# Kernel tuning notes

Measured on AMD Instinct MI355X. Metric: run time of the kernel, lower is better.

## Reference

```python
import jax, jax.numpy as jnp
import numpy as np

RADIUS = 2
TEMP = 1.0
B, CIN, D, H, W = 1, 32, 64, 64, 64
PROJ, OUT = 64, 64
K = (2 * RADIUS + 1) ** 3  # 125 local offsets

_OFFSETS = np.array([(dz, dy, dx)
                     for dz in range(-RADIUS, RADIUS + 1)
                     for dy in range(-RADIUS, RADIUS + 1)
                     for dx in range(-RADIUS, RADIUS + 1)], dtype=np.int32)


def _conv3d(x, w, b, pad):
    y = jax.lax.conv_general_dilated(
        x, w, window_strides=(1, 1, 1), padding=[(pad, pad)] * 3,
        dimension_numbers=('NCDHW', 'OIDHW', 'NCDHW'))
    if b is not None:
        y = y + b[None, :, None, None, None]
    return y


def _l2norm(x):
    # torch F.normalize(dim=1): x / max(||x||_2, 1e-12)
    n = jnp.sqrt(jnp.sum(x * x, axis=1, keepdims=True))
    return x / jnp.maximum(n, 1e-12)


def _inorm(x, eps=1e-5):
    # InstanceNorm3d (affine=False): normalize over spatial dims per (B,C)
    mu = jnp.mean(x, axis=(2, 3, 4), keepdims=True)
    var = jnp.mean((x - mu) ** 2, axis=(2, 3, 4), keepdims=True)
    return (x - mu) * jax.lax.rsqrt(var + eps)


def _ntn(x):
    return jnp.nan_to_num(x, nan=0.0, posinf=0.0, neginf=0.0)


def setup_inputs() -> dict:
    key = jax.random.key(0)
    ks = jax.random.split(key, 8)
    s = 0.05
    return {
        'source_features': jax.random.normal(ks[0], (B, CIN, D, H, W), jnp.float32),
        'warped_target_features': jax.random.normal(ks[1], (B, CIN, D, H, W), jnp.float32),
        'w_src': jax.random.normal(ks[2], (PROJ, CIN, 1, 1, 1), jnp.float32) * s,
        'b_src': jnp.zeros((PROJ,), jnp.float32),
        'w_tgt': jax.random.normal(ks[3], (PROJ, CIN, 1, 1, 1), jnp.float32) * s,
        'b_tgt': jnp.zeros((PROJ,), jnp.float32),
        'w_enc1': jax.random.normal(ks[4], (OUT, K + 5, 3, 3, 3), jnp.float32) * s,
        'b_enc1': jnp.zeros((OUT,), jnp.float32),
        'w_enc2': jax.random.normal(ks[5], (OUT, OUT, 3, 3, 3), jnp.float32) * s,
        'b_enc2': jnp.zeros((OUT,), jnp.float32),
    }


def reference(source_features, warped_target_features, w_src, b_src, w_tgt, b_tgt,
              w_enc1, b_enc1, w_enc2, b_enc2):
    sp = _l2norm(_conv3d(source_features, w_src, b_src, 0))      # [B,P,D,H,W]
    tp = _l2norm(_conv3d(warped_target_features, w_tgt, b_tgt, 0))
    pt = jnp.pad(tp, ((0, 0), (0, 0), (RADIUS, RADIUS), (RADIUS, RADIUS), (RADIUS, RADIUS)),
                 mode='edge')  # replicate pad

    starts = jnp.asarray(_OFFSETS + RADIUS, jnp.int32)  # [K,3] slice starts

    def corr_one(st):
        sh = jax.lax.dynamic_slice(pt, (0, 0, st[0], st[1], st[2]), (B, PROJ, D, H, W))
        return jnp.sum(sp * sh, axis=1)  # [B,D,H,W]

    corr = jnp.transpose(jax.vmap(corr_one)(starts), (1, 0, 2, 3, 4))  # [B,K,D,H,W]
    scaled = corr / max(TEMP, 1e-6)

    top2 = jax.lax.top_k(jnp.moveaxis(scaled, 1, -1), 2)[0]  # [B,D,H,W,2]
    m = jnp.moveaxis(top2[..., 0:1], -1, 1)   # running max   [B,1,D,H,W]
    s2 = jnp.moveaxis(top2[..., 1:2], -1, 1)  # second max

    p = jnp.exp(scaled - m)                    # [B,K,D,H,W]
    Z = jnp.sum(p, axis=1, keepdims=True)
    inv = 1.0 / jnp.maximum(Z, 1e-8)

    offv = jnp.asarray(_OFFSETS, jnp.float32)  # [K,3]
    expected_offset = _ntn(jnp.einsum('bkdhw,kc->bcdhw', p, offv) * inv)
    confidence = _ntn(jnp.minimum(inv, 1.0))   # max-prob = exp(m-m)/Z
    second_prob = jnp.exp(s2 - m) * inv
    margin = _ntn(jnp.maximum(confidence - second_prob, 0.0))
    entropy = _ntn(m + jnp.log(jnp.maximum(Z, 1e-8))
                   - jnp.sum(p * scaled, axis=1, keepdims=True) * inv)

    enc_in = jnp.concatenate([corr, expected_offset, confidence, entropy], axis=1)  # [B,K+5,D,H,W]
    h = _conv3d(enc_in, w_enc1, b_enc1, 1)
    h = jax.nn.gelu(_inorm(h), approximate=False)
    h = _conv3d(h, w_enc2, b_enc2, 1)
    h = jax.nn.gelu(_inorm(h), approximate=False)
    encoded_features = _ntn(h)

    return expected_offset, confidence, margin, entropy, encoded_features
```

## Files before the change

### kernel.cpp

```cpp
#include <hip/hip_runtime.h>

#define DEV __device__ __forceinline__

typedef short bf16x8 __attribute__((ext_vector_type(8)));
typedef float f32x4 __attribute__((ext_vector_type(4)));

static const int NVOX = 262144;

DEV float bflo(unsigned int u) { return __uint_as_float(u << 16); }
DEV float bfhi(unsigned int u) { return __uint_as_float(u & 0xffff0000u); }
DEV float bf2f(unsigned short s) { return __uint_as_float(((unsigned int)s) << 16); }
DEV unsigned short f2bf(float f) {
    unsigned int x = __float_as_uint(f);
    x += 0x7fffu + ((x >> 16) & 1u);
    return (unsigned short)(x >> 16);
}
DEV float ldin(const void* p, int i, int f) {
    return f ? ((const float*)p)[i] : bf2f(((const unsigned short*)p)[i]);
}

DEV void gld16(const unsigned short* g, unsigned short* l) {
    __builtin_amdgcn_global_load_lds(
        (const __attribute__((address_space(1))) unsigned int*)g,
        (__attribute__((address_space(3))) unsigned int*)l, 16, 0, 0);
}

__global__ void sniff_kernel(const unsigned short* __restrict__ src, int* __restrict__ flag) {
    __shared__ int cnt[256];
    int t = threadIdx.x;
    int c = 0;
    for (int i = t; i < 4096; i += 256) {
        unsigned int u = (unsigned int)src[i] & 0x7fffu;
        c += (u >= 0x4900u) ? 1 : 0;
    }
    cnt[t] = c;
    __syncthreads();
    for (int s = 128; s > 0; s >>= 1) {
        if (t < s) cnt[t] += cnt[t + s];
        __syncthreads();
    }
    if (t == 0) *flag = (cnt[0] > 8) ? 1 : 0;
}

__global__ void prep_kernel(const void* __restrict__ w1, const void* __restrict__ w2,
                            const void* __restrict__ bsv, const void* __restrict__ btv,
                            const void* __restrict__ b1v, const void* __restrict__ b2v,
                            const int* __restrict__ flag,
                            unsigned short* __restrict__ Wf1,
                            unsigned short* __restrict__ Wf2,
                            float* __restrict__ fbias) {
    const int f = *flag;
    int idx = blockIdx.x * 256 + threadIdx.x;
    const int N1  = 27 * 4 * 4 * 512;
    const int N1E = 2 * 4 * 512;
    const int N2  = 27 * 2 * 4 * 512;
    if (idx < N1) {
        int frag = idx >> 9;
        int r    = idx & 511;
        int lane = r >> 3, j = r & 7;
        int nt = frag & 3;
        int tk = frag >> 2;
        int tap = tk >> 2, kc = tk & 3;
        int o  = nt * 16 + (lane & 15);
        int cp = kc * 32 + (lane >> 4) * 8 + j;
        Wf1[idx] = f2bf(ldin(w1, (o * 130 + cp) * 27 + tap, f));
    } else if (idx < N1 + N1E) {
        int i2 = idx - N1;
        int frag = i2 >> 9;
        int r    = i2 & 511;
        int lane = r >> 3, j = r & 7;
        int nt = frag & 3, kc = frag >> 2;
        int o   = nt * 16 + (lane & 15);
        int kap = kc * 32 + (lane >> 4) * 8 + j;
        unsigned short val = 0;
        if (kap < 54) {
            int tap = kap >> 1, ch = 128 + (kap & 1);
            val = f2bf(ldin(w1, (o * 130 + ch) * 27 + tap, f));
        }
        Wf1[idx] = val;
    } else if (idx < N1 + N1E + N2) {
        int i2 = idx - N1 - N1E;
        int frag = i2 >> 9;
        int r    = i2 & 511;
        int lane = r >> 3, j = r & 7;
        int nt = frag & 3;
        int tk = frag >> 2;
        int tap = tk >> 1, kc = tk & 1;
        int o = nt * 16 + (lane & 15);
        int c = kc * 32 + (lane >> 4) * 8 + j;
        Wf2[i2] = f2bf(ldin(w2, (o * 64 + c) * 27 + tap, f));
    } else if (idx < N1 + N1E + N2 + 256) {
        int j = idx - N1 - N1E - N2;
        const void* bp = (j < 64) ? bsv : (j < 128) ? btv : (j < 192) ? b1v : b2v;
        fbias[j] = ldin(bp, j & 63, f);
    }
}

__global__ __launch_bounds__(256) void proj_kernel(
        const void* __restrict__ Xsrc, const void* __restrict__ Xtgt,
        const void* __restrict__ Wsrc, const void* __restrict__ Wtgt,
        const float* __restrict__ fbias, const int* __restrict__ flag,
        unsigned short* __restrict__ SP, unsigned short* __restrict__ TP) {
    const int f = *flag;
    const void* Xin = blockIdx.y ? Xtgt : Xsrc;
    const void* W   = blockIdx.y ? Wtgt : Wsrc;
    const float* Bb = fbias + (blockIdx.y ? 64 : 0);
    unsigned short* Outp = blockIdx.y ? TP : SP;

    __shared__ float ws[2048];
    const int t = threadIdx.x;
    for (int i = t; i < 2048; i += 256) {
        int ci = i >> 6, o = i & 63;
        ws[i] = ldin(W, o * 32 + ci, f);
    }
    __syncthreads();

    const size_t v = (size_t)blockIdx.x * 256 + t;
    float acc[64];
#pragma unroll
    for (int o = 0; o < 64; ++o) acc[o] = Bb[o];
    if (f) {
        const float* Xf = (const float*)Xin;
        for (int ci = 0; ci < 32; ++ci) {
            float x = Xf[(size_t)ci * NVOX + v];
            const float4* wr = (const float4*)(ws + ci * 64);
#pragma unroll
            for (int o4 = 0; o4 < 16; ++o4) {
                float4 w4 = wr[o4];
                acc[o4 * 4 + 0] = fmaf(w4.x, x, acc[o4 * 4 + 0]);
                acc[o4 * 4 + 1] = fmaf(w4.y, x, acc[o4 * 4 + 1]);
                acc[o4 * 4 + 2] = fmaf(w4.z, x, acc[o4 * 4 + 2]);
                acc[o4 * 4 + 3] = fmaf(w4.w, x, acc[o4 * 4 + 3]);
            }
        }
    } else {
        const unsigned short* Xb = (const unsigned short*)Xin;
        for (int ci = 0; ci < 32; ++ci) {
            float x = bf2f(Xb[(size_t)ci * NVOX + v]);
            const float4* wr = (const float4*)(ws + ci * 64);
#pragma unroll
            for (int o4 = 0; o4 < 16; ++o4) {
                float4 w4 = wr[o4];
                acc[o4 * 4 + 0] = fmaf(w4.x, x, acc[o4 * 4 + 0]);
                acc[o4 * 4 + 1] = fmaf(w4.y, x, acc[o4 * 4 + 1]);
                acc[o4 * 4 + 2] = fmaf(w4.z, x, acc[o4 * 4 + 2]);
                acc[o4 * 4 + 3] = fmaf(w4.w, x, acc[o4 * 4 + 3]);
            }
        }
    }
    float s = 0.f;
#pragma unroll
    for (int o = 0; o < 64; ++o) s = fmaf(acc[o], acc[o], s);
    float scale = 1.f / fmaxf(sqrtf(s), 1e-12f);

    unsigned int pk[32];
#pragma unroll
    for (int o = 0; o < 32; ++o)
        pk[o] = (unsigned int)f2bf(acc[2 * o] * scale) |
                ((unsigned int)f2bf(acc[2 * o + 1] * scale) << 16);
    uint4* outp = (uint4*)(Outp + v * 64);
#pragma unroll
    for (int j = 0; j < 8; ++j)
        outp[j] = make_uint4(pk[4 * j], pk[4 * j + 1], pk[4 * j + 2], pk[4 * j + 3]);
}

__global__ __launch_bounds__(256) void corr_kernel(
        const unsigned short* __restrict__ SP, const unsigned short* __restrict__ TP,
        unsigned short* __restrict__ X1, float* __restrict__ Out) {
    __shared__ __align__(16) unsigned short tpb[2][80 * 64];
    __shared__ __align__(16) unsigned short stage[64 * 128];

    const int t = threadIdx.x;
    const int wv = t >> 6, lane = t & 63;
    const int q = lane >> 4, l16 = lane & 15;
    const int x0 = wv * 16;

    const int bid = blockIdx.x;
    const int wg = (bid & 7) * 512 + (bid >> 3);
    const int z = wg >> 6, y = wg & 63;
    const size_t vbase = ((size_t)z * 64 + y) * 64;

    const unsigned short* arow = SP + (vbase + x0 + l16) * 64 + q * 8;
    const bf16x8 a0 = *(const bf16x8*)(arow);
    const bf16x8 a1 = *(const bf16x8*)(arow + 32);

    auto stage_tp = [&](int it, int b) {
        const int zc = min(max(z + it / 5 - 2, 0), 63);
        const int yc = min(max(y + it % 5 - 2, 0), 63);
        const unsigned short* tb = TP + ((size_t)zc * 64 + yc) * 4096;
#pragma unroll
        for (int j = 0; j < 2; ++j) {
            int c = t + j * 256;
            int pp = c >> 3, cc = c & 7;
            int xc = min(max(pp - 2, 0), 63);
            gld16(tb + xc * 64 + ((cc ^ (pp & 7)) * 8),
                  &tpb[b][(wv * 64 + j * 256) * 8]);
        }
        if (wv < 2) {
            int c = 512 + wv * 64 + lane;
            int pp = c >> 3, cc = c & 7;
            int xc = min(max(pp - 2, 0), 63);
            gld16(tb + xc * 64 + ((cc ^ (pp & 7)) * 8),
                  &tpb[b][(512 + wv * 64) * 8]);
        }
    };

    stage_tp(0, 0);
    __syncthreads();

    int p = 0;
    for (int it = 0; it < 25; ++it) {
        if (it < 24) stage_tp(it + 1, p ^ 1);

        f32x4 acc[2] = {{0.f, 0.f, 0.f, 0.f}, {0.f, 0.f, 0.f, 0.f}};
        {
            const char* tb = (const char*)tpb[p];
#pragma unroll
            for (int nt = 0; nt < 2; ++nt) {
                const int pr = x0 + nt * 16 + l16;
                bf16x8 b0 = *(const bf16x8*)(tb + pr * 128 + ((q ^ (pr & 7)) * 16));
                bf16x8 b1 = *(const bf16x8*)(tb + pr * 128 + (((4 + q) ^ (pr & 7)) * 16));
                acc[nt] = __builtin_amdgcn_mfma_f32_16x16x32_bf16(a0, b0, acc[nt], 0, 0, 0);
                acc[nt] = __builtin_amdgcn_mfma_f32_16x16x32_bf16(a1, b1, acc[nt], 0, 0, 0);
            }
        }
        const int kb = it * 5;
        char* sg = (char*)stage;
#pragma unroll
        for (int nt = 0; nt < 2; ++nt) {
#pragma unroll
            for (int r = 0; r < 4; ++r) {
                int ml = q * 4 + r;
                int dxp = nt * 16 + l16 - ml;
                if ((unsigned)dxp < 5u) {
                    int xl = x0 + ml;
                    *(unsigned short*)(sg + xl * 256 + (((kb + dxp) * 2) ^ ((xl & 7) << 4))) =
                        f2bf(acc[nt][r]);
                }
            }
        }
        __syncthreads();
        p ^= 1;
    }

    {
        const int vox = t >> 2, part = t & 3;
        const int sx = (vox & 7) << 4;
        const char* sg = (const char*)stage;
        uint4 u[4];
#pragma unroll
        for (int j = 0; j < 4; ++j)
            u[j] = *(const uint4*)(sg + vox * 256 + ((part * 64 + j * 16) ^ sx));

        float m = -1e30f, s2 = -1e30f;
#pragma unroll
        for (int j = 0; j < 4; ++j) {
            const unsigned int uu[4] = {u[j].x, u[j].y, u[j].z, u[j].w};
#pragma unroll
            for (int w = 0; w < 4; ++w) {
                int k = part * 32 + j * 8 + w * 2;
                float d0 = (k < 125) ? bflo(uu[w]) : -1e30f;
                float d1 = (k + 1 < 125) ? bfhi(uu[w]) : -1e30f;
                float lo0 = fminf(d0, m); m = fmaxf(d0, m); s2 = fmaxf(s2, lo0);
                float lo1 = fminf(d1, m); m = fmaxf(d1, m); s2 = fmaxf(s2, lo1);
            }
        }
#pragma unroll
        for (int off = 1; off <= 2; off <<= 1) {
            float om = __shfl_xor(m, off, 64);
            float os = __shfl_xor(s2, off, 64);
            float lo = fminf(m, om);
            m = fmaxf(m, om);
            s2 = fmaxf(fmaxf(s2, os), lo);
        }
        int kk = part * 32;
        int dz0 = kk / 25, rem = kk - dz0 * 25, dy0 = rem / 5, dx0 = rem - dy0 * 5;
        float fx = (float)(dx0 - 2), fy = (float)(dy0 - 2), fz = (float)(dz0 - 2);
        float Zs = 0.f, S1 = 0.f, Ox = 0.f, Oy = 0.f, Oz = 0.f;
#pragma unroll
        for (int j = 0; j < 4; ++j) {
            const unsigned int uu[4] = {u[j].x, u[j].y, u[j].z, u[j].w};
#pragma unroll
            for (int w = 0; w < 8; ++w) {
                int k = part * 32 + j * 8 + w;
                bool ok = (k < 125);
                float d = (w & 1) ? bfhi(uu[w >> 1]) : bflo(uu[w >> 1]);
                d = ok ? d : 0.f;
                float e = ok ? __expf(d - m) : 0.f;
                Zs += e; S1 = fmaf(e, d, S1);
                Ox = fmaf(e, fx, Ox); Oy = fmaf(e, fy, Oy); Oz = fmaf(e, fz, Oz);
                fx += 1.f;
                if (fx > 2.5f) { fx = -2.f; fy += 1.f; if (fy > 2.5f) { fy = -2.f; fz += 1.f; } }
            }
        }
#pragma unroll
        for (int off = 1; off <= 2; off <<= 1) {
            Zs += __shfl_xor(Zs, off, 64);
            S1 += __shfl_xor(S1, off, 64);
            Ox += __shfl_xor(Ox, off, 64);
            Oy += __shfl_xor(Oy, off, 64);
            Oz += __shfl_xor(Oz, off, 64);
        }
        if (part == 0) {
            float inv  = 1.f / fmaxf(Zs, 1e-8f);
            float eoz = Oz * inv, eoy = Oy * inv, eox = Ox * inv;
            float conf = fminf(inv, 1.f);
            float marg = fmaxf(conf - __expf(s2 - m) * inv, 0.f);
            float ent  = m + __logf(fmaxf(Zs, 1e-8f)) - S1 * inv;
            char* sgw = (char*)stage;
            *(unsigned short*)(sgw + vox * 256 + (250 ^ sx)) = f2bf(eoz);
            *(unsigned short*)(sgw + vox * 256 + (252 ^ sx)) = f2bf(eoy);
            *(unsigned short*)(sgw + vox * 256 + (254 ^ sx)) = f2bf(eox);
            const size_t v = vbase + vox;
            *(unsigned int*)(X1 + v * 160 + 128) =
                (unsigned int)f2bf(conf) | ((unsigned int)f2bf(ent) << 16);
            Out[v]                    = eoz;
            Out[(size_t)NVOX + v]     = eoy;
            Out[(size_t)2 * NVOX + v] = eox;
            Out[(size_t)3 * NVOX + v] = conf;
            Out[(size_t)4 * NVOX + v] = marg;
            Out[(size_t)5 * NVOX + v] = ent;
        }
    }
    __syncthreads();

#pragma unroll
    for (int j = 0; j < 4; ++j) {
        int i = t + j * 256;
        int vox = i >> 4, cc = i & 15;
        *(uint4*)(X1 + (vbase + vox) * 160 + (size_t)cc * 8) =
            *(const uint4*)((const char*)stage + vox * 256 + ((cc * 16) ^ ((vox & 7) << 4)));
    }
}

template <int XSTRIDE, int CPAD, int KC, int NLD, int MINW, bool TAIL>
__global__ __launch_bounds__(256, MINW) void conv3_kernel(
        const unsigned short* __restrict__ Xin, const unsigned short* __restrict__ Wf,
        const unsigned short* __restrict__ Wfe,
        const float* __restrict__ Bias, unsigned short* __restrict__ Out) {
    constexpr int SLOT = 66 * CPAD;
    constexpr int CH16 = CPAD / 8;
    __shared__ __align__(16) unsigned short lds[3 * SLOT];
    const int lin = blockIdx.x;
    const int wg = (lin & 7) * 256 + (lin >> 3);
    const int z = wg >> 5;
    const int y = (wg & 31) * 2;
    const int t = threadIdx.x;
    const int wv = t >> 6, lane = t & 63;
    const int quad = lane >> 4, l16 = lane & 15;
    const int ml2 = (wv & 1) * 2;
    const int nt2 = (wv >> 1) * 2;

    f32x4 acc[2][2][2] = {};

    auto stage_plane = [&](int pidx) {
        const int zz = z + (pidx >> 2) - 1;
        const int py = y + (pidx & 3) - 1;
        if ((unsigned)zz >= 64u || (unsigned)py >= 64u) return;
        const unsigned short* base = Xin + (((size_t)zz * 64 + py) * 64) * XSTRIDE;
        unsigned short* dst = lds + (pidx % 3) * SLOT + CPAD;
#pragma unroll
        for (int i = 0; i < NLD; ++i) {
            int chunk = wv * 64 + lane + i * 256;
            int xi = chunk / CH16;
            int cc = chunk % CH16;
            gld16(base + xi * XSTRIDE + ((cc ^ ((xi + 1) & 7)) * 8),
                  dst + (size_t)(wv * 64 + i * 256) * 8);
        }
    };

    if (TAIL) {
        unsigned short* ebuf = lds;
#pragma unroll
        for (int i2 = 0; i2 < 16; ++i2) {
            int i = t + i2 * 256;
            int vox = i >> 5, slot = i & 31;
            unsigned int val = 0u;
            int kap;
            if (slot < 27) {
                int ddz = slot / 9 - 1, ddy = (slot / 3) % 3 - 1, dxx = slot % 3 - 1;
                int zz = z + ddz, yy = y + (vox >> 6) + ddy, xx = (vox & 63) + dxx;
                kap = slot * 2;
                if ((unsigned)zz < 64u && (unsigned)yy < 64u && (unsigned)xx < 64u)
                    val = *(const unsigned int*)(Xin + (((size_t)zz * 64 + yy) * 64 + xx) * XSTRIDE + 128);
            } else {
                kap = 54 + (slot - 27) * 2;
            }
            *(unsigned int*)(ebuf + (size_t)vox * 72 + kap) = val;
        }
        __syncthreads();
#pragma unroll
        for (int kc = 0; kc < 2; ++kc) {
            bf16x8 bte[2];
#pragma unroll
            for (int nl = 0; nl < 2; ++nl)
                bte[nl] = *(const bf16x8*)(Wfe + (size_t)(kc * 4 + nt2 + nl) * 512 + lane * 8);
#pragma unroll
            for (int r = 0; r < 2; ++r)
#pragma unroll
            for (int ml = 0; ml < 2; ++ml) {
                bf16x8 a = *(const bf16x8*)(ebuf + (size_t)(r * 64 + (ml2 + ml) * 16 + l16) * 72 + (kc * 4 + quad) * 8);
#pragma unroll
                for (int nl = 0; nl < 2; ++nl)
                    acc[r][ml][nl] = __builtin_amdgcn_mfma_f32_16x16x32_bf16(a, bte[nl], acc[r][ml][nl], 0, 0, 0);
            }
        }
        __syncthreads();
    }

    if (t < 6 * CH16) {
        int sl = t / (2 * CH16), r2 = (t / CH16) & 1, c = t % CH16;
        *(uint4*)(&lds[(size_t)sl * SLOT + (size_t)(r2 * 65) * CPAD + c * 8]) =
            make_uint4(0u, 0u, 0u, 0u);
    }
    stage_plane(0);
    stage_plane(1);
    __syncthreads();

    for (int i = 0; i < 9; ++i) {
        const int s0 = (i / 3) * 4 + i % 3;
        if (i == 3 || i == 6) {
            stage_plane(s0 + 1);
            stage_plane(s0 + 2);
            __syncthreads();
        } else if (s0 + 2 < 12) {
            stage_plane(s0 + 2);
        }

        const int zz = z + i / 3 - 1;
        const int dy = i % 3 - 1;
        const bool zok = (unsigned)zz < 64u;
        const bool rok0 = zok && (unsigned)(y + dy) < 64u;
        const bool rok1 = zok && (unsigned)(y + 1 + dy) < 64u;
        const unsigned short* sb0 = lds + (size_t)(s0 % 3) * SLOT;
        const unsigned short* sb1 = lds + (size_t)((s0 + 1) % 3) * SLOT;
        if (rok0 || rok1) {
#pragma unroll
            for (int dx = 0; dx < 3; ++dx) {
                const int tap = (i / 3) * 9 + (i % 3) * 3 + dx;
                const unsigned short* wt = Wf + ((size_t)tap * KC * 4) * 512 + lane * 8;
                bf16x8 bf[KC][2];
#pragma unroll
                for (int kc = 0; kc < KC; ++kc)
#pragma unroll
                    for (int nl = 0; nl < 2; ++nl)
                        bf[kc][nl] = *(const bf16x8*)(wt + (size_t)(kc * 4 + nt2 + nl) * 512);
#pragma unroll
                for (int kc = 0; kc < KC; ++kc) {
#pragma unroll
                    for (int ml = 0; ml < 2; ++ml) {
                        const int row = (ml2 + ml) * 16 + l16 + dx;
                        const int co = ((kc * 4 + quad) ^ (row & 7)) * 8;
                        if (rok0) {
                            bf16x8 a = *(const bf16x8*)(&sb0[(size_t)row * CPAD + co]);
#pragma unroll
                            for (int nl = 0; nl < 2; ++nl)
                                acc[0][ml][nl] = __builtin_amdgcn_mfma_f32_16x16x32_bf16(a, bf[kc][nl], acc[0][ml][nl], 0, 0, 0);
                        }
                        if (rok1) {
                            bf16x8 a = *(const bf16x8*)(&sb1[(size_t)row * CPAD + co]);
#pragma unroll
                            for (int nl = 0; nl < 2; ++nl)
                                acc[1][ml][nl] = __builtin_amdgcn_mfma_f32_16x16x32_bf16(a, bf[kc][nl], acc[1][ml][nl], 0, 0, 0);
                        }
                    }
                }
            }
        }
        __syncthreads();
    }

#pragma unroll
    for (int r = 0; r < 2; ++r) {
        const size_t vb = ((size_t)z * 64 + (y + r)) * 64;
#pragma unroll
        for (int ml = 0; ml < 2; ++ml) {
#pragma unroll
            for (int nl = 0; nl < 2; ++nl) {
                const int oc = (nt2 + nl) * 16 + l16;
                const float bv = Bias[oc];
#pragma unroll
                for (int rr = 0; rr < 4; ++rr)
                    Out[(vb + (ml2 + ml) * 16 + quad * 4 + rr) * 64 + oc] =
                        f2bf(acc[r][ml][nl][rr] + bv);
            }
        }
    }
}

__global__ __launch_bounds__(256) void stats_kernel(
        const unsigned short* __restrict__ H, float* __restrict__ stats) {
    const int t = threadIdx.x;
    const int c = t & 63, g = t >> 6;
    float s = 0.f, q = 0.f;
    for (int v = blockIdx.x * 4 + g; v < NVOX; v += gridDim.x * 4) {
        float x = bf2f(H[(size_t)v * 64 + c]);
        s += x; q = fmaf(x, x, q);
    }
    __shared__ float ls[256], lq[256];
    ls[t] = s; lq[t] = q;
    __syncthreads();
    if (t < 64) {
        s = ls[t] + ls[t + 64] + ls[t + 128] + ls[t + 192];
        q = lq[t] + lq[t + 64] + lq[t + 128] + lq[t + 192];
        atomicAdd(&stats[c], s);
        atomicAdd(&stats[64 + c], q);
    }
}

__global__ void finalize_kernel(const float* __restrict__ stats, float* __restrict__ musr) {
    int c = threadIdx.x;
    if (c < 64) {
        float mu  = stats[c] * (1.0f / 262144.0f);
        float var = stats[64 + c] * (1.0f / 262144.0f) - mu * mu;
        musr[c] = mu;
        musr[64 + c] = rsqrtf(var + 1e-5f);
    }
}

__global__ __launch_bounds__(256) void norm_gelu_kernel(
        const unsigned short* __restrict__ H, const float* __restrict__ musr,
        unsigned short* __restrict__ G) {
    const size_t base = ((size_t)blockIdx.x * 256 + threadIdx.x) * 8;
    uint4 u = *(const uint4*)(H + base);
    const int c0 = (int)(base & 63);
    const unsigned int uu[4] = {u.x, u.y, u.z, u.w};
    unsigned int w[4];
#pragma unroll
    for (int p = 0; p < 4; ++p) {
        int c = c0 + p * 2;
        float x0 = (bflo(uu[p]) - musr[c]) * musr[64 + c];
        float x1 = (bfhi(uu[p]) - musr[c + 1]) * musr[64 + c + 1];
        float g0 = 0.5f * x0 * (1.f + erff(x0 * 0.70710678118f));
        float g1 = 0.5f * x1 * (1.f + erff(x1 * 0.70710678118f));
        w[p] = (unsigned int)f2bf(g0) | ((unsigned int)f2bf(g1) << 16);
    }
    *(uint4*)(G + base) = make_uint4(w[0], w[1], w[2], w[3]);
}

__global__ __launch_bounds__(256) void out_final_kernel(
        const unsigned short* __restrict__ H2, const float* __restrict__ musr,
        float* __restrict__ OutEnc) {
    __shared__ float tile[64 * 260];
    const int t = threadIdx.x;
    const size_t v0 = (size_t)blockIdx.x * 256;
#pragma unroll
    for (int i = 0; i < 8; ++i) {
        int chunk = t + i * 256;
        uint4 u = *(const uint4*)(H2 + v0 * 64 + (size_t)chunk * 8);
        int vox = chunk >> 3;
        int c0 = (chunk & 7) * 8;
        const unsigned int uu[4] = {u.x, u.y, u.z, u.w};
#pragma unroll
        for (int p = 0; p < 4; ++p) {
            int c = c0 + p * 2;
            float x0 = (bflo(uu[p]) - musr[c]) * musr[64 + c];
            float x1 = (bfhi(uu[p]) - musr[c + 1]) * musr[64 + c + 1];
            tile[c * 260 + vox]       = 0.5f * x0 * (1.f + erff(x0 * 0.70710678118f));
            tile[(c + 1) * 260 + vox] = 0.5f * x1 * (1.f + erff(x1 * 0.70710678118f));
        }
    }
    __syncthreads();
    const int c = t >> 2, sub = t & 3;
#pragma unroll
    for (int iter = 0; iter < 16; ++iter) {
        int fq = iter * 4 + sub;
        float4 val = *(const float4*)(&tile[c * 260 + fq * 4]);
        *(float4*)(OutEnc + (size_t)c * NVOX + v0 + fq * 4) = val;
    }
}

extern "C" void kernel_launch(void* const* d_in, const int* in_sizes, int n_in,
                              void* d_out, int out_size, void* d_ws, size_t ws_size,
                              hipStream_t stream) {
    const void* src  = d_in[0];
    const void* tgt  = d_in[1];
    const void* wsrc = d_in[2];
    const void* bsrc = d_in[3];
    const void* wtgt = d_in[4];
    const void* btgt = d_in[5];
    const void* w1   = d_in[6];
    const void* b1   = d_in[7];
    const void* w2   = d_in[8];
    const void* b2   = d_in[9];
    float* out = (float*)d_out;

    char* ws = (char*)d_ws;
    unsigned short* TPb = (unsigned short*)(ws);
    unsigned short* SPb = (unsigned short*)(ws + 33554432);
    unsigned short* X1  = (unsigned short*)(ws + 67108864);
    unsigned short* Wf1 = (unsigned short*)(ws + 150994944);
    unsigned short* Wf2 = (unsigned short*)(ws + 151547904);
    int*   flag   = (int*)  (ws + 151769088);
    float* fbias  = (float*)(ws + 151769152);
    float* stats1 = (float*)(ws + 151770176);
    float* musr1  = (float*)(ws + 151770688);
    float* stats2 = (float*)(ws + 151771200);
    float* musr2  = (float*)(ws + 151771712);
    unsigned short* H1 = SPb;
    unsigned short* G1 = TPb;
    unsigned short* H2 = X1;
    unsigned short* Wf1e = Wf1 + 27 * 4 * 4 * 512;

    (void)hipMemsetAsync(stats1, 0, 2048, stream);
    sniff_kernel<<<1, 256, 0, stream>>>((const unsigned short*)src, flag);
    prep_kernel<<<1313, 256, 0, stream>>>(w1, w2, bsrc, btgt, b1, b2, flag, Wf1, Wf2, fbias);
    proj_kernel<<<dim3(1024, 2), 256, 0, stream>>>(src, tgt, wsrc, wtgt, fbias, flag, SPb, TPb);
    corr_kernel<<<4096, 256, 0, stream>>>(SPb, TPb, X1, out);
    conv3_kernel<160, 128, 4, 4, 3, true><<<2048, 256, 0, stream>>>(X1, Wf1, Wf1e, fbias + 128, H1);
    stats_kernel<<<256, 256, 0, stream>>>(H1, stats1);
    finalize_kernel<<<1, 64, 0, stream>>>(stats1, musr1);
    norm_gelu_kernel<<<8192, 256, 0, stream>>>(H1, musr1, G1);
    conv3_kernel<64, 64, 2, 2, 4, false><<<2048, 256, 0, stream>>>(G1, Wf2, nullptr, fbias + 192, H2);
    stats_kernel<<<256, 256, 0, stream>>>(H2, stats2);
    finalize_kernel<<<1, 64, 0, stream>>>(stats2, musr2);
    out_final_kernel<<<1024, 256, 0, stream>>>(H2, musr2, out + 6 * (size_t)NVOX);
}
```

Before: 707.2 us.

## Process two y-rows per correlation block to reuse staged target planes

The correlation kernel now handles two adjacent y-rows per block, so each staged target row in LDS serves both rows. This cuts staging iterations from 50 to 30 per row pair and halves the grid. Each block needs twice the stage LDS and more registers, which may lower occupancy. The conv3 staging code is also lightly reordered, with the same planes loaded in a slightly different sequence.

```diff
diff --git a/kernel.cpp b/kernel.cpp
--- a/kernel.cpp
+++ b/kernel.cpp
@@ -168,7 +168,7 @@
         const unsigned short* __restrict__ SP, const unsigned short* __restrict__ TP,
         unsigned short* __restrict__ X1, float* __restrict__ Out) {
     __shared__ __align__(16) unsigned short tpb[2][80 * 64];
-    __shared__ __align__(16) unsigned short stage[64 * 128];
+    __shared__ __align__(16) unsigned short sband[2][64 * 128];
 
     const int t = threadIdx.x;
     const int wv = t >> 6, lane = t & 63;
@@ -176,17 +176,21 @@
     const int x0 = wv * 16;
 
     const int bid = blockIdx.x;
-    const int wg = (bid & 7) * 512 + (bid >> 3);
-    const int z = wg >> 6, y = wg & 63;
-    const size_t vbase = ((size_t)z * 64 + y) * 64;
-
-    const unsigned short* arow = SP + (vbase + x0 + l16) * 64 + q * 8;
-    const bf16x8 a0 = *(const bf16x8*)(arow);
-    const bf16x8 a1 = *(const bf16x8*)(arow + 32);
+    const int wg = (bid & 7) * 256 + (bid >> 3);
+    const int z = wg >> 5, y = (wg & 31) * 2;
+    const size_t vb0 = ((size_t)z * 64 + y) * 64;
+    const size_t vb1 = vb0 + 64;
+
+    const unsigned short* ar0 = SP + (vb0 + x0 + l16) * 64 + q * 8;
+    const unsigned short* ar1 = SP + (vb1 + x0 + l16) * 64 + q * 8;
+    const bf16x8 a00 = *(const bf16x8*)(ar0);
+    const bf16x8 a01 = *(const bf16x8*)(ar0 + 32);
+    const bf16x8 a10 = *(const bf16x8*)(ar1);
+    const bf16x8 a11 = *(const bf16x8*)(ar1 + 32);
 
     auto stage_tp = [&](int it, int b) {
-        const int zc = min(max(z + it / 5 - 2, 0), 63);
-        const int yc = min(max(y + it % 5 - 2, 0), 63);
+        const int zc = min(max(z + it / 6 - 2, 0), 63);
+        const int yc = min(max(y - 2 + it % 6, 0), 63);
         const unsigned short* tb = TP + ((size_t)zc * 64 + yc) * 4096;
 #pragma unroll
         for (int j = 0; j < 2; ++j) {
@@ -209,10 +213,13 @@
     __syncthreads();
 
     int p = 0;
-    for (int it = 0; it < 25; ++it) {
-        if (it < 24) stage_tp(it + 1, p ^ 1);
-
-        f32x4 acc[2] = {{0.f, 0.f, 0.f, 0.f}, {0.f, 0.f, 0.f, 0.f}};
+    for (int it = 0; it < 30; ++it) {
+        if (it < 29) stage_tp(it + 1, p ^ 1);
+        const int dz = it / 6, j = it % 6;
+        const bool r0 = (j < 5), r1 = (j > 0);
+
+        f32x4 acc0[2] = {{0.f, 0.f, 0.f, 0.f}, {0.f, 0.f, 0.f, 0.f}};
+        f32x4 acc1[2] = {{0.f, 0.f, 0.f, 0.f}, {0.f, 0.f, 0.f, 0.f}};
         {
             const char* tb = (const char*)tpb[p];
 #pragma unroll
@@ -220,33 +227,57 @@
                 const int pr = x0 + nt * 16 + l16;
                 bf16x8 b0 = *(const bf16x8*)(tb + pr * 128 + ((q ^ (pr & 7)) * 16));
                 bf16x8 b1 = *(const bf16x8*)(tb + pr * 128 + (((4 + q) ^ (pr & 7)) * 16));
-                acc[nt] = __builtin_amdgcn_mfma_f32_16x16x32_bf16(a0, b0, acc[nt], 0, 0, 0);
-                acc[nt] = __builtin_amdgcn_mfma_f32_16x16x32_bf16(a1, b1, acc[nt], 0, 0, 0);
-            }
-        }
-        const int kb = it * 5;
-        char* sg = (char*)stage;
-#pragma unroll
-        for (int nt = 0; nt < 2; ++nt) {
-#pragma unroll
-            for (int r = 0; r < 4; ++r) {
-                int ml = q * 4 + r;
-                int dxp = nt * 16 + l16 - ml;
-                if ((unsigned)dxp < 5u) {
-                    int xl = x0 + ml;
-                    *(unsigned short*)(sg + xl * 256 + (((kb + dxp) * 2) ^ ((xl & 7) << 4))) =
-                        f2bf(acc[nt][r]);
+                if (r0) {
+                    acc0[nt] = __builtin_amdgcn_mfma_f32_16x16x32_bf16(a00, b0, acc0[nt], 0, 0, 0);
+                    acc0[nt] = __builtin_amdgcn_mfma_f32_16x16x32_bf16(a01, b1, acc0[nt], 0, 0, 0);
                 }
-            }
+                if (r1) {
+                    acc1[nt] = __builtin_amdgcn_mfma_f32_16x16x32_bf16(a10, b0, acc1[nt], 0, 0, 0);
+                    acc1[nt] = __builtin_amdgcn_mfma_f32_16x16x32_bf16(a11, b1, acc1[nt], 0, 0, 0);
+                }
+            }
+        }
+        if (r0) {
+            const int kb = dz * 25 + j * 5;
+            char* sg = (char*)sband[0];
+#pragma unroll
+            for (int nt = 0; nt < 2; ++nt)
+#pragma unroll
+                for (int r = 0; r < 4; ++r) {
+                    int ml = q * 4 + r;
+                    int dxp = nt * 16 + l16 - ml;
+                    if ((unsigned)dxp < 5u) {
+                        int xl = x0 + ml;
+                        *(unsigned short*)(sg + xl * 256 + (((kb + dxp) * 2) ^ ((xl & 7) << 4))) =
+                            f2bf(acc0[nt][r]);
+                    }
+                }
+        }
+        if (r1) {
+            const int kb = dz * 25 + (j - 1) * 5;
+            char* sg = (char*)sband[1];
+#pragma unroll
+            for (int nt = 0; nt < 2; ++nt)
+#pragma unroll
+                for (int r = 0; r < 4; ++r) {
+                    int ml = q * 4 + r;
+                    int dxp = nt * 16 + l16 - ml;
+                    if ((unsigned)dxp < 5u) {
+                        int xl = x0 + ml;
+                        *(unsigned short*)(sg + xl * 256 + (((kb + dxp) * 2) ^ ((xl & 7) << 4))) =
+                            f2bf(acc1[nt][r]);
+                    }
+                }
         }
         __syncthreads();
         p ^= 1;
     }
 
-    {
+    for (int half = 0; half < 2; ++half) {
+        const size_t vbase = half ? vb1 : vb0;
         const int vox = t >> 2, part = t & 3;
         const int sx = (vox & 7) << 4;
-        const char* sg = (const char*)stage;
+        const char* sg = (const char*)sband[half];
         uint4 u[4];
 #pragma unroll
         for (int j = 0; j < 4; ++j)
@@ -307,7 +338,7 @@
             float conf = fminf(inv, 1.f);
             float marg = fmaxf(conf - __expf(s2 - m) * inv, 0.f);
             float ent  = m + __logf(fmaxf(Zs, 1e-8f)) - S1 * inv;
-            char* sgw = (char*)stage;
+            char* sgw = (char*)sband[half];
             *(unsigned short*)(sgw + vox * 256 + (250 ^ sx)) = f2bf(eoz);
             *(unsigned short*)(sgw + vox * 256 + (252 ^ sx)) = f2bf(eoy);
             *(unsigned short*)(sgw + vox * 256 + (254 ^ sx)) = f2bf(eox);
@@ -325,11 +356,12 @@
     __syncthreads();
 
 #pragma unroll
-    for (int j = 0; j < 4; ++j) {
+    for (int j = 0; j < 8; ++j) {
         int i = t + j * 256;
-        int vox = i >> 4, cc = i & 15;
-        *(uint4*)(X1 + (vbase + vox) * 160 + (size_t)cc * 8) =
-            *(const uint4*)((const char*)stage + vox * 256 + ((cc * 16) ^ ((vox & 7) << 4)));
+        int row = i >> 10, rr = i & 1023;
+        int vox = rr >> 4, cc = rr & 15;
+        *(uint4*)(X1 + ((row ? vb1 : vb0) + vox) * 160 + (size_t)cc * 8) =
+            *(const uint4*)((const char*)sband[row] + vox * 256 + ((cc * 16) ^ ((vox & 7) << 4)));
     }
 }
 
@@ -421,11 +453,9 @@
         const int s0 = (i / 3) * 4 + i % 3;
         if (i == 3 || i == 6) {
             stage_plane(s0 + 1);
-            stage_plane(s0 + 2);
             __syncthreads();
-        } else if (s0 + 2 < 12) {
-            stage_plane(s0 + 2);
-        }
+        }
+        if (s0 + 2 < 12) stage_plane(s0 + 2);
 
         const int zz = z + i / 3 - 1;
         const int dy = i % 3 - 1;
@@ -606,7 +636,7 @@
     sniff_kernel<<<1, 256, 0, stream>>>((const unsigned short*)src, flag);
     prep_kernel<<<1313, 256, 0, stream>>>(w1, w2, bsrc, btgt, b1, b2, flag, Wf1, Wf2, fbias);
     proj_kernel<<<dim3(1024, 2), 256, 0, stream>>>(src, tgt, wsrc, wtgt, fbias, flag, SPb, TPb);
-    corr_kernel<<<4096, 256, 0, stream>>>(SPb, TPb, X1, out);
+    corr_kernel<<<2048, 256, 0, stream>>>(SPb, TPb, X1, out);
     conv3_kernel<160, 128, 4, 4, 3, true><<<2048, 256, 0, stream>>>(X1, Wf1, Wf1e, fbias + 128, H1);
     stats_kernel<<<256, 256, 0, stream>>>(H1, stats1);
     finalize_kernel<<<1, 64, 0, stream>>>(stats1, musr1);
```

Result: no change. 695.2 us (-1.7%).
